# Kernel tuning notes

Hardware: AMD Instinct MI355X
Metric: run time of the kernel (lower is better)

Reference implementation:

```python
import jax, jax.numpy as jnp
import numpy as np

EPS = 1e-8


def _conv1d(x, w, b):
    # x: [B, E, L], w: [F, E, K], b: [F] -> [B, F, L] (k=3, pad=1 keeps length)
    y = jax.lax.conv_general_dilated(
        x, w, window_strides=(1,), padding=[(1, 1)],
        dimension_numbers=("NCH", "OIH", "NCH"))
    return y + b[None, :, None]


def setup_inputs() -> dict:
    key = jax.random.key(0)
    kq, ka, ke, kw, kb, ku = jax.random.split(key, 6)
    B, QL, AL = 512, 128, 512
    V, E, F, K = 50000, 300, 400, 3
    question = jax.random.randint(kq, (B, QL), 0, V + 1, dtype=jnp.int64)
    answer = jax.random.randint(ka, (B, AL), 0, V + 1, dtype=jnp.int64)
    emb_table = jax.random.normal(ke, (V + 1, E), dtype=jnp.float32)
    emb_table = emb_table.at[0].set(0.0)  # padding_idx=0
    conv_w = jax.random.normal(kw, (F, E, K), dtype=jnp.float32) * 0.05
    conv_b = jax.random.normal(kb, (F,), dtype=jnp.float32) * 0.05
    U = jax.random.normal(ku, (F, F), dtype=jnp.float32) * 0.1
    return {"question": question, "answer": answer, "emb_table": emb_table,
            "conv_w": conv_w, "conv_b": conv_b, "U": U}


def reference(question, answer, emb_table, conv_w, conv_b, U):
    q = emb_table[question]              # [B, QL, E]
    a = emb_table[answer]                # [B, AL, E]
    Q = _conv1d(q.transpose(0, 2, 1), conv_w, conv_b)   # [B, F, QL]
    A = _conv1d(a.transpose(0, 2, 1), conv_w, conv_b)   # [B, F, AL]
    # G = tanh(Q^T U A): [B, QL, AL]
    G = jnp.tanh(jnp.einsum("bfq,fg,bga->bqa", Q, U, A))
    roQ = jax.nn.softmax(jnp.max(G, axis=2), axis=1)    # [B, QL]
    roA = jax.nn.softmax(jnp.max(G, axis=1), axis=1)    # [B, AL]
    rQ = jnp.einsum("bfq,bq->bf", Q, roQ)               # [B, F]
    rA = jnp.einsum("bfa,ba->bf", A, roA)               # [B, F]
    nQ = jnp.maximum(jnp.linalg.norm(rQ, axis=1), EPS)
    nA = jnp.maximum(jnp.linalg.norm(rA, axis=1), EPS)
    return jnp.sum(rQ * rA, axis=1) / (nQ * nA)         # [B]
```

## Files before the change

kernel.cpp:

```cpp
#include <hip/hip_runtime.h>
#include <math.h>

typedef unsigned int   uint32;
typedef unsigned short ushort16;
typedef __attribute__((ext_vector_type(8))) short  short8;
typedef __attribute__((ext_vector_type(4))) float  floatx4;

#define Bb   512
#define QLn  128
#define ALn  512
#define En   300
#define Fn   400
#define OW   416
#define EPAD 320
#define NV   50001
#define ECROWS 50176
#define ECSTRIDE 2560

typedef const __attribute__((address_space(1))) unsigned int guint_t;
typedef __attribute__((address_space(3))) unsigned int luint_t;
#define GLDS16(g, l) __builtin_amdgcn_global_load_lds((guint_t*)(g), (luint_t*)(l), 16, 0, 0)

static __device__ __forceinline__ float bf_lo(uint32 u) { return __uint_as_float(u << 16); }
static __device__ __forceinline__ float bf_hi(uint32 u) { return __uint_as_float(u & 0xffff0000u); }
static __device__ __forceinline__ ushort16 f2bf(float f) {
    uint32 u = __float_as_uint(f);
    uint32 r = (u + 0x7fffu + ((u >> 16) & 1u)) >> 16;
    return (ushort16)r;
}
static __device__ __forceinline__ uint32 pack2(float a, float b) {
    return (uint32)f2bf(a) | ((uint32)f2bf(b) << 16);
}

__global__ __launch_bounds__(128) void embcvt_kernel(
        const float* __restrict__ emb, char* __restrict__ embbf)
{
    const int r = blockIdx.x, j = threadIdx.x;
    const float* er = emb + (size_t)r * En;
    uint32* orow = (uint32*)(embbf + (size_t)r * 640);
    for (int d = j; d < 160; d += 128) {
        uint32 v = 0;
        if (d < 150) {
            float2 f2v = *(const float2*)(er + 2 * d);
            v = pack2(f2v.x, f2v.y);
        }
        orow[d] = v;
    }
}

__global__ __launch_bounds__(256) void prep_wt(
        const float* __restrict__ W, const float* __restrict__ cb,
        ushort16* __restrict__ Wt2, float* __restrict__ bias2)
{
    const int f = blockIdx.x, t = threadIdx.x;
    for (int p2 = t; p2 < 480; p2 += 256) {
        int p = 2 * p2;
        float v0 = 0.f, v1 = 0.f;
        if (f < Fn) {
            int kk = p / EPAD, e = p - kk * EPAD;
            if (e < En)     v0 = W[(size_t)f * 900 + e * 3 + kk];
            if (e + 1 < En) v1 = W[(size_t)f * 900 + (e + 1) * 3 + kk];
        }
        *(uint32*)&Wt2[(size_t)f * 960 + p] = pack2(v0, v1);
    }
    if (t == 0) bias2[f] = (f < Fn) ? cb[f] : 0.f;
}

__global__ __launch_bounds__(256) void prep_ub(
        const float* __restrict__ U, ushort16* __restrict__ Ub)
{
    const int g = blockIdx.x, t = threadIdx.x;
    uint32* orow = (uint32*)(Ub + (size_t)g * 416);
    for (int f2 = t; f2 < 208; f2 += 256) {
        int f = 2 * f2;
        float v0 = 0.f, v1 = 0.f;
        if (g < Fn) {
            if (f < Fn)     v0 = U[(size_t)f * Fn + g];
            if (f + 1 < Fn) v1 = U[(size_t)(f + 1) * Fn + g];
        }
        orow[f2] = pack2(v0, v1);
    }
}

__global__ __launch_bounds__(512) void ec_gemm(
        const char* __restrict__ embbf, const char* __restrict__ Wt2,
        char* __restrict__ EC)
{
    __shared__ __align__(16) char As[32768];
    __shared__ __align__(16) char Bs[32768];
    const int bx = blockIdx.x;
    const int g = bx / 40, rem = bx - g * 40;
    const int c = rem >> 3, vt = g * 8 + (rem & 7);
    if (vt >= 196) return;
    const int t = threadIdx.x, lane = t & 63, w = t >> 6;
    const int v0 = vt * 256, c0 = c * 256;
    const int wr = w >> 2, wc = w & 3;
    const int fm = lane & 15;
    const int cg = ((lane & 3) - ((lane >> 3) & 3)) & 3;
    const int rl = lane >> 2;
    const int chunkOff = (((lane >> 4) + (fm >> 1)) & 3) * 16;

    const char* srcA[2];
    const char* srcB[2];
#pragma unroll
    for (int i = 0; i < 2; ++i) {
        srcA[i] = embbf + (size_t)(v0 + w * 32 + i * 16 + rl) * 640 + cg * 16;
        int n = c0 + w * 32 + i * 16 + rl;
        int kk = n / 416, f = n - kk * 416;
        if (n >= 1248) { kk = 0; f = 508; }
        srcB[i] = Wt2 + (size_t)f * 1920 + kk * 640 + cg * 16;
    }
    char* AsW = As + w * 2048;
    char* BsW = Bs + w * 2048;

    floatx4 acc[8][4];
    const floatx4 zz = {0.f, 0.f, 0.f, 0.f};
#pragma unroll
    for (int m = 0; m < 8; ++m)
#pragma unroll
        for (int n = 0; n < 4; ++n) acc[m][n] = zz;

#define ESTG(ko, buf) do {                                                    \
        const int _ko = (ko); const int _bo = (buf) * 16384;                  \
        GLDS16(srcA[0] + _ko, AsW + _bo);                                     \
        GLDS16(srcA[1] + _ko, AsW + _bo + 1024);                              \
        GLDS16(srcB[0] + _ko, BsW + _bo);                                     \
        GLDS16(srcB[1] + _ko, BsW + _bo + 1024);                              \
    } while (0)

    int cur = 0;
    ESTG(0, 0);
    __syncthreads();
    for (int ks = 0; ks < 10; ++ks) {
        const int nxt = cur ^ 1;
        if (ks < 9) ESTG((ks + 1) * 64, nxt);
        short8 af[8], bfv[4];
        const char* Ac = As + cur * 16384;
        const char* Bc = Bs + cur * 16384;
#pragma unroll
        for (int m = 0; m < 8; ++m)
            af[m] = *(const short8*)(Ac + (wr * 128 + m * 16 + fm) * 64 + chunkOff);
#pragma unroll
        for (int n = 0; n < 4; ++n)
            bfv[n] = *(const short8*)(Bc + (wc * 64 + n * 16 + fm) * 64 + chunkOff);
        __builtin_amdgcn_s_setprio(1);
#pragma unroll
        for (int m = 0; m < 8; ++m)
#pragma unroll
            for (int n = 0; n < 4; ++n)
                acc[m][n] = __builtin_amdgcn_mfma_f32_16x16x32_bf16(
                    bfv[n], af[m], acc[m][n], 0, 0, 0);
        __builtin_amdgcn_s_setprio(0);
        __syncthreads();
        cur = nxt;
    }
#undef ESTG

#pragma unroll
    for (int m = 0; m < 8; ++m) {
        const int v = v0 + wr * 128 + m * 16 + fm;
#pragma unroll
        for (int n = 0; n < 4; ++n) {
            const int f0 = c0 + wc * 64 + n * 16 + ((lane >> 4) * 4);
            uint2 o;
            o.x = pack2(acc[m][n][0], acc[m][n][1]);
            o.y = pack2(acc[m][n][2], acc[m][n][3]);
            *(uint2*)(EC + (size_t)v * ECSTRIDE + f0 * 2) = o;
        }
    }
}

static __device__ __forceinline__ void gather_one(
        const int* __restrict__ toks, const char* __restrict__ EC,
        const float* __restrict__ bias2, char* __restrict__ outb,
        int id, int L)
{
    const uint32 uid = (uint32)id;
    const int c = (int)(uid % 52u);
    const int r = (int)(uid / 52u);
    const int l = r & (L - 1), b = r / L;
    const int* tr = toks + (size_t)b * L;
    const int t0 = (l > 0)     ? tr[l - 1] : 0;
    const int t1 = tr[l];
    const int t2 = (l < L - 1) ? tr[l + 1] : 0;
    const uint4 x0 = *(const uint4*)(EC + (size_t)t0 * ECSTRIDE +        c * 16);
    const uint4 x1 = *(const uint4*)(EC + (size_t)t1 * ECSTRIDE +  832 + c * 16);
    const uint4 x2 = *(const uint4*)(EC + (size_t)t2 * ECSTRIDE + 1664 + c * 16);
    const float4 b0 = *(const float4*)(bias2 + c * 8);
    const float4 b1 = *(const float4*)(bias2 + c * 8 + 4);
    uint4 o;
    o.x = pack2(bf_lo(x0.x) + bf_lo(x1.x) + bf_lo(x2.x) + b0.x,
                bf_hi(x0.x) + bf_hi(x1.x) + bf_hi(x2.x) + b0.y);
    o.y = pack2(bf_lo(x0.y) + bf_lo(x1.y) + bf_lo(x2.y) + b0.z,
                bf_hi(x0.y) + bf_hi(x1.y) + bf_hi(x2.y) + b0.w);
    o.z = pack2(bf_lo(x0.z) + bf_lo(x1.z) + bf_lo(x2.z) + b1.x,
                bf_hi(x0.z) + bf_hi(x1.z) + bf_hi(x2.z) + b1.y);
    o.w = pack2(bf_lo(x0.w) + bf_lo(x1.w) + bf_lo(x2.w) + b1.z,
                bf_hi(x0.w) + bf_hi(x1.w) + bf_hi(x2.w) + b1.w);
    *(uint4*)(outb + (size_t)r * 832 + c * 16) = o;
}

#define GQB 1024
#define GAB 4096
__global__ __launch_bounds__(256) void gather_both(
        const int* __restrict__ question, const int* __restrict__ answer,
        const char* __restrict__ EC, const float* __restrict__ bias2,
        char* __restrict__ qb, char* __restrict__ ab, int nb)
{
    const int bx = blockIdx.x, t = threadIdx.x;
    if (bx < GQB) {
        const int total = nb * QLn * 52;
        for (int id = bx * 256 + t; id < total; id += GQB * 256)
            gather_one(question, EC, bias2, qb, id, QLn);
    } else {
        const int total = nb * ALn * 52;
        for (int id = (bx - GQB) * 256 + t; id < total; id += GAB * 256)
            gather_one(answer, EC, bias2, ab, id, ALn);
    }
}

template<int NWM, int NWN, int MF, int NF, int BR>
static __device__ __forceinline__ void qp_tile(
        const char* __restrict__ Qb, const char* __restrict__ Ub,
        char* __restrict__ ob, int col0, char* As, char* Bs)
{
    const int t = threadIdx.x, lane = t & 63, w = t >> 6;
    const int wr = w / NWN, wc = w % NWN;
    const int fm = lane & 15;
    const int cg = ((lane & 3) - ((lane >> 3) & 3)) & 3;
    const int rl = lane >> 2;
    const int chunkOff = (((lane >> 4) + (fm >> 1)) & 3) * 16;

    const char* srcA = Qb + (size_t)(w * 16 + rl) * 832 + cg * 16;
    const char* srcB0; const char* srcB1 = 0;
    if (BR == 256) {
        srcB0 = Ub + (size_t)(col0 + w * 32 + rl) * 832 + cg * 16;
        srcB1 = srcB0 + (size_t)16 * 832;
    } else {
        srcB0 = Ub + (size_t)(col0 + w * 16 + rl) * 832 + cg * 16;
        srcB1 = Ub + (size_t)(col0 + 128 + w * 16 + rl) * 832 + cg * 16;
    }
    char* AsW = As + w * 1024;
    char* BsW0; char* BsW1;
    if (BR == 256) { BsW0 = Bs + w * 2048; BsW1 = BsW0 + 1024; }
    else           { BsW0 = Bs + w * 1024; BsW1 = Bs + 8192 + w * 1024; }
    const int BUFB = BR * 64;

    floatx4 acc[MF][NF];
    const floatx4 zz = {0.f, 0.f, 0.f, 0.f};
#pragma unroll
    for (int m = 0; m < MF; ++m)
#pragma unroll
        for (int n = 0; n < NF; ++n) acc[m][n] = zz;

#define QSTG(ko, buf) do {                                                    \
        const int _ko = (ko);                                                 \
        GLDS16(srcA + _ko, AsW + (buf) * 8192);                               \
        GLDS16(srcB0 + _ko, BsW0 + (buf) * BUFB);                             \
        if (BR == 256 || w < 2) GLDS16(srcB1 + _ko, BsW1 + (buf) * BUFB);     \
    } while (0)

    int cur = 0;
    QSTG(0, 0);
    __syncthreads();
    for (int ks = 0; ks < 13; ++ks) {
        const int nxt = cur ^ 1;
        if (ks < 12) QSTG((ks + 1) * 64, nxt);
        short8 af[MF], bfv[NF];
        const char* Ac = As + cur * 8192;
        const char* Bc = Bs + cur * BUFB;
#pragma unroll
        for (int m = 0; m < MF; ++m)
            af[m] = *(const short8*)(Ac + (wr * (MF * 16) + m * 16 + fm) * 64 + chunkOff);
#pragma unroll
        for (int n = 0; n < NF; ++n)
            bfv[n] = *(const short8*)(Bc + (wc * (NF * 16) + n * 16 + fm) * 64 + chunkOff);
        __builtin_amdgcn_s_setprio(1);
#pragma unroll
        for (int m = 0; m < MF; ++m)
#pragma unroll
            for (int n = 0; n < NF; ++n)
                acc[m][n] = __builtin_amdgcn_mfma_f32_16x16x32_bf16(
                    af[m], bfv[n], acc[m][n], 0, 0, 0);
        __builtin_amdgcn_s_setprio(0);
        __syncthreads();
        cur = nxt;
    }
#undef QSTG

#pragma unroll
    for (int m = 0; m < MF; ++m) {
        const int row = wr * (MF * 16) + m * 16 + ((lane >> 4) * 4);
#pragma unroll
        for (int n = 0; n < NF; ++n) {
            const int col = col0 + wc * (NF * 16) + n * 16 + fm;
#pragma unroll
            for (int r = 0; r < 4; ++r)
                *(ushort16*)(ob + (size_t)(row + r) * 832 + col * 2) =
                    f2bf(acc[m][n][r]);
        }
    }
}

__global__ __launch_bounds__(512) void qp_gemm(
        const char* __restrict__ qb, const char* __restrict__ Ub,
        char* __restrict__ qpb, int nb)
{
    __shared__ __align__(16) char As[16384];
    __shared__ __align__(16) char Bs[32768];
    const int bx = blockIdx.x;
    const int xcd = bx & 7, rest = bx >> 3;
    const int nt = rest & 1, b = (rest >> 1) * 8 + xcd;
    if (b >= nb) return;
    const char* Qb = qb + (size_t)b * 106496;
    char* ob = qpb + (size_t)b * 106496;
    if (nt == 0)
        qp_tile<2, 4, 4, 4, 256>(Qb, Ub, ob, 0, As, Bs);
    else
        qp_tile<4, 2, 2, 5, 160>(Qb, Ub, ob, 256, As, Bs);
}

__global__ __launch_bounds__(256) void fused_g(
        const ushort16* __restrict__ Qp,
        const ushort16* __restrict__ Av,
        float* __restrict__ rowPart,
        float* __restrict__ colMg,
        int nb)
{
    __shared__ __align__(16) char Qs[16384];
    __shared__ __align__(16) char Asl[32768];
    __shared__ float rowM4[128][4];

    const int t = threadIdx.x, lane = t & 63, w = t >> 6;
    const int bx = blockIdx.x;
    const int xcd = bx & 7, rest = bx >> 3;
    const int c = rest & 1, b = (rest >> 1) * 8 + xcd;
    if (b >= nb) return;
    const int fm = lane & 15;
    const int cg = ((lane & 3) - ((lane >> 3) & 3)) & 3;
    const int rl = lane >> 2;
    const int chunkOff = (((lane >> 4) + (fm >> 1)) & 3) * 16;

    const char* Qpb = (const char*)Qp + (size_t)b * 106496;
    const char* Ab  = (const char*)Av + (size_t)b * 425984 + (size_t)c * 212992;
    const char* srcQ0 = Qpb + (size_t)(w * 16 + rl) * 832 + cg * 16;
    const char* srcQ1 = Qpb + (size_t)(64 + w * 16 + rl) * 832 + cg * 16;
    const char* srcA0 = Ab  + (size_t)(w * 64 + rl) * 832 + cg * 16;

    floatx4 acc[8][4];
    const floatx4 zz = {0.f, 0.f, 0.f, 0.f};
#pragma unroll
    for (int m = 0; m < 8; ++m)
#pragma unroll
        for (int n = 0; n < 4; ++n) acc[m][n] = zz;

#define FSTG(ko, buf) do {                                                    \
        const int _ko = (ko);                                                 \
        GLDS16(srcQ0 + _ko, Qs + (buf) * 8192 + w * 1024);                    \
        GLDS16(srcQ1 + _ko, Qs + (buf) * 8192 + 4096 + w * 1024);             \
        GLDS16(srcA0 + _ko,         Asl + (buf) * 16384 + w * 4096);          \
        GLDS16(srcA0 + 13312 + _ko, Asl + (buf) * 16384 + w * 4096 + 1024);   \
        GLDS16(srcA0 + 26624 + _ko, Asl + (buf) * 16384 + w * 4096 + 2048);   \
        GLDS16(srcA0 + 39936 + _ko, Asl + (buf) * 16384 + w * 4096 + 3072);   \
    } while (0)

    int cur = 0;
    FSTG(0, 0);
    __syncthreads();

    for (int ks = 0; ks < 13; ++ks) {
        const int nxt = cur ^ 1;
        if (ks < 12) FSTG((ks + 1) * 64, nxt);

        short8 qa[8], aa_[4];
        const char* Qc = Qs + cur * 8192;
        const char* Ac = Asl + cur * 16384;
#pragma unroll
        for (int m = 0; m < 8; ++m)
            qa[m] = *(const short8*)(Qc + (m * 16 + fm) * 64 + chunkOff);
#pragma unroll
        for (int n = 0; n < 4; ++n)
            aa_[n] = *(const short8*)(Ac + (w * 64 + n * 16 + fm) * 64 + chunkOff);
        __builtin_amdgcn_s_setprio(1);
#pragma unroll
        for (int m = 0; m < 8; ++m)
#pragma unroll
            for (int n = 0; n < 4; ++n)
                acc[m][n] = __builtin_amdgcn_mfma_f32_16x16x32_bf16(
                    qa[m], aa_[n], acc[m][n], 0, 0, 0);
        __builtin_amdgcn_s_setprio(0);
        __syncthreads();
        cur = nxt;
    }
#undef FSTG

#pragma unroll
    for (int m = 0; m < 8; ++m)
#pragma unroll
        for (int r = 0; r < 4; ++r) {
            float v = fmaxf(fmaxf(acc[m][0][r], acc[m][1][r]),
                            fmaxf(acc[m][2][r], acc[m][3][r]));
            v = fmaxf(v, __shfl_xor(v, 1));
            v = fmaxf(v, __shfl_xor(v, 2));
            v = fmaxf(v, __shfl_xor(v, 4));
            v = fmaxf(v, __shfl_xor(v, 8));
            if (fm == 0) rowM4[m * 16 + (lane >> 4) * 4 + r][w] = v;
        }
#pragma unroll
    for (int n = 0; n < 4; ++n) {
        float v = -1e30f;
#pragma unroll
        for (int m = 0; m < 8; ++m)
#pragma unroll
            for (int r = 0; r < 4; ++r) v = fmaxf(v, acc[m][n][r]);
        v = fmaxf(v, __shfl_xor(v, 16));
        v = fmaxf(v, __shfl_xor(v, 32));
        if (lane < 16)
            colMg[(size_t)b * 512 + c * 256 + w * 64 + n * 16 + lane] = v;
    }
    __syncthreads();
    if (t < 128)
        rowPart[((size_t)b * 2 + c) * 128 + t] =
            fmaxf(fmaxf(rowM4[t][0], rowM4[t][1]),
                  fmaxf(rowM4[t][2], rowM4[t][3]));
}

static __device__ __forceinline__ float block_reduce_max_1k(float v, volatile float* red) {
    int t = threadIdx.x;
    red[t] = v; __syncthreads();
    for (int s = 512; s > 0; s >>= 1) {
        if (t < s) red[t] = fmaxf(red[t], red[t + s]);
        __syncthreads();
    }
    float r = red[0]; __syncthreads();
    return r;
}
static __device__ __forceinline__ float block_reduce_sum_1k(float v, volatile float* red) {
    int t = threadIdx.x;
    red[t] = v; __syncthreads();
    for (int s = 512; s > 0; s >>= 1) {
        if (t < s) red[t] = red[t] + red[t + s];
        __syncthreads();
    }
    float r = red[0]; __syncthreads();
    return r;
}

__global__ __launch_bounds__(1024) void fused_pool(
        const ushort16* __restrict__ Qv,
        const ushort16* __restrict__ Av,
        const float* __restrict__ rowPart,
        const float* __restrict__ colMg,
        float* __restrict__ out)
{
    __shared__ float colv[ALn];
    __shared__ float roq[QLn];
    __shared__ float red[1024];
    __shared__ float part[4][4][208];
    const int t = threadIdx.x, b = blockIdx.x;

    float v = -1e30f;
    if (t < QLn) {
        const float* rp = rowPart + (size_t)b * 256;
        v = tanhf(fmaxf(rp[t], rp[128 + t]));
    }
    float vmax = block_reduce_max_1k(v, red);
    float ex = (t < QLn) ? __expf(v - vmax) : 0.f;
    float ssum = block_reduce_sum_1k(ex, red);
    if (t < QLn) roq[t] = ex / ssum;

    float cv = (t < ALn) ? tanhf(colMg[(size_t)b * 512 + t]) : -1e30f;
    float cmax = block_reduce_max_1k(cv, red);
    float e0 = (t < ALn) ? __expf(cv - cmax) : 0.f;
    float csum = block_reduce_sum_1k(e0, red);
    if (t < ALn) colv[t] = e0 / csum;
    __syncthreads();

    if (t < 832) {
        const int h = t / 208, c = t - h * 208;
        float rq0 = 0.f, rq1 = 0.f, ra0 = 0.f, ra1 = 0.f;
        const uint32* Qb32 = (const uint32*)((const char*)Qv + (size_t)b * 106496);
#pragma unroll 4
        for (int q = h * 32; q < h * 32 + 32; ++q) {
            float wv = roq[q];
            uint32 u = Qb32[q * 208 + c];
            rq0 = fmaf(bf_lo(u), wv, rq0);
            rq1 = fmaf(bf_hi(u), wv, rq1);
        }
        const uint32* Ab32 = (const uint32*)((const char*)Av + (size_t)b * 425984);
#pragma unroll 4
        for (int a = h * 128; a < h * 128 + 128; ++a) {
            float wv = colv[a];
            uint32 u = Ab32[a * 208 + c];
            ra0 = fmaf(bf_lo(u), wv, ra0);
            ra1 = fmaf(bf_hi(u), wv, ra1);
        }
        part[0][h][c] = rq0; part[1][h][c] = rq1;
        part[2][h][c] = ra0; part[3][h][c] = ra1;
    }
    __syncthreads();

    float dd = 0.f, qq = 0.f, aam = 0.f;
    if (t < 208) {
        float q0 = part[0][0][t] + part[0][1][t] + part[0][2][t] + part[0][3][t];
        float q1 = part[1][0][t] + part[1][1][t] + part[1][2][t] + part[1][3][t];
        float a0 = part[2][0][t] + part[2][1][t] + part[2][2][t] + part[2][3][t];
        float a1 = part[3][0][t] + part[3][1][t] + part[3][2][t] + part[3][3][t];
        dd  = q0 * a0 + q1 * a1;
        qq  = q0 * q0 + q1 * q1;
        aam = a0 * a0 + a1 * a1;
    }
    dd  = block_reduce_sum_1k(dd, red);
    qq  = block_reduce_sum_1k(qq, red);
    aam = block_reduce_sum_1k(aam, red);
    if (t == 0) {
        float nq = fmaxf(sqrtf(qq), 1e-8f);
        float na = fmaxf(sqrtf(aam), 1e-8f);
        out[b] = dd / (nq * na);
    }
}

extern "C" void kernel_launch(void* const* d_in, const int* in_sizes, int n_in,
                              void* d_out, int out_size, void* d_ws, size_t ws_size,
                              hipStream_t stream)
{
    const int*   question = (const int*)d_in[0];
    const int*   answer   = (const int*)d_in[1];
    const float* emb      = (const float*)d_in[2];
    const float* conv_w   = (const float*)d_in[3];
    const float* conv_b   = (const float*)d_in[4];
    const float* U        = (const float*)d_in[5];
    float* out = (float*)d_out;
    char* ws = (char*)d_ws;

    const size_t WT2B   = (size_t)512 * 960 * 2;
    const size_t UBB    = (size_t)416 * 416 * 2;
    const size_t ECB    = (size_t)ECROWS * ECSTRIDE;
    const size_t FIXED0 = WT2B + 2048 + UBB + ECB;
    const size_t QB     = (size_t)QLn * OW * 2;
    const size_t AB     = (size_t)ALn * OW * 2;
    const size_t MXB    = 4096;
    const size_t PER_B  = 2 * QB + AB + MXB;

    size_t avail = (ws_size > FIXED0) ? (ws_size - FIXED0) : 0;
    int CB = (int)(avail / PER_B);
    if (CB > Bb) CB = Bb;
    if (CB < 1)  CB = 1;
    int nch = (Bb + CB - 1) / CB;
    int CBe = (Bb + nch - 1) / nch;

    char*  wt2   = ws;
    float* bias2 = (float*)(ws + WT2B);
    char*  ub    = ws + WT2B + 2048;
    char*  EC    = ws + WT2B + 2048 + UBB;
    char*  embbf = ws + FIXED0;
    char*  qb    = ws + FIXED0;
    char*  qpb   = qb  + (size_t)CB * QB;
    char*  ab    = qpb + (size_t)CB * QB;
    float* rowP  = (float*)(ab + (size_t)CB * AB);
    float* colM  = rowP + (size_t)CB * 512;

    embcvt_kernel<<<NV, 128, 0, stream>>>(emb, embbf);
    prep_wt<<<512, 256, 0, stream>>>(conv_w, conv_b, (ushort16*)wt2, bias2);
    prep_ub<<<416, 256, 0, stream>>>(U, (ushort16*)ub);
    ec_gemm<<<1000, 512, 0, stream>>>(embbf, wt2, EC);

    for (int b0 = 0; b0 < Bb; b0 += CBe) {
        int nb = (Bb - b0 < CBe) ? (Bb - b0) : CBe;
        int nb8 = (nb + 7) / 8;
        gather_both<<<GQB + GAB, 256, 0, stream>>>(
            question + (size_t)b0 * QLn, answer + (size_t)b0 * ALn,
            EC, bias2, qb, ab, nb);
        qp_gemm<<<nb8 * 16, 512, 0, stream>>>(qb, ub, qpb, nb);
        fused_g<<<nb8 * 16, 256, 0, stream>>>((const ushort16*)qpb, (const ushort16*)ab,
                                              rowP, colM, nb);
        fused_pool<<<nb, 1024, 0, stream>>>((const ushort16*)qb, (const ushort16*)ab,
                                            rowP, colM, out + b0);
    }
}
```

Before: 610.3 us.

## Triple-buffer ec_gemm loads with explicit waitcnt and widen gather per thread

The embedding-conv GEMM moves from double to triple buffering in LDS (96KB). It uses explicit vmcnt waits and a single barrier per k-step, so global-to-LDS loads run two stages ahead and one barrier per iteration is dropped. The grid changes from a grouped 1D launch to a plain 2D launch, which loses the earlier block ordering meant for L2 reuse. The gather kernel now processes two 16-byte chunks per thread instead of one. The larger LDS footprint may lower occupancy.

After: 615.7 us. No clear change (+0.9%).

```diff
diff --git a/kernel.cpp b/kernel.cpp
--- a/kernel.cpp
+++ b/kernel.cpp
@@ -86,12 +86,9 @@
         const char* __restrict__ embbf, const char* __restrict__ Wt2,
         char* __restrict__ EC)
 {
-    __shared__ __align__(16) char As[32768];
-    __shared__ __align__(16) char Bs[32768];
-    const int bx = blockIdx.x;
-    const int g = bx / 40, rem = bx - g * 40;
-    const int c = rem >> 3, vt = g * 8 + (rem & 7);
-    if (vt >= 196) return;
+    __shared__ __align__(16) char As[49152];
+    __shared__ __align__(16) char Bs[49152];
+    const int vt = blockIdx.x, c = blockIdx.y;
     const int t = threadIdx.x, lane = t & 63, w = t >> 6;
     const int v0 = vt * 256, c0 = c * 256;
     const int wr = w >> 2, wc = w & 3;
@@ -128,21 +125,28 @@
         GLDS16(srcB[1] + _ko, BsW + _bo + 1024);                              \
     } while (0)
 
-    int cur = 0;
     ESTG(0, 0);
-    __syncthreads();
+    ESTG(64, 1);
+
+#pragma unroll
     for (int ks = 0; ks < 10; ++ks) {
-        const int nxt = cur ^ 1;
-        if (ks < 9) ESTG((ks + 1) * 64, nxt);
+        if (ks == 9) asm volatile("s_waitcnt vmcnt(0)" ::: "memory");
+        else         asm volatile("s_waitcnt vmcnt(4)" ::: "memory");
+        __builtin_amdgcn_s_barrier();
+        __builtin_amdgcn_sched_barrier(0);
+
         short8 af[8], bfv[4];
-        const char* Ac = As + cur * 16384;
-        const char* Bc = Bs + cur * 16384;
+        const char* Ac = As + (ks % 3) * 16384;
+        const char* Bc = Bs + (ks % 3) * 16384;
 #pragma unroll
         for (int m = 0; m < 8; ++m)
             af[m] = *(const short8*)(Ac + (wr * 128 + m * 16 + fm) * 64 + chunkOff);
 #pragma unroll
         for (int n = 0; n < 4; ++n)
             bfv[n] = *(const short8*)(Bc + (wc * 64 + n * 16 + fm) * 64 + chunkOff);
+
+        if (ks < 8) ESTG((ks + 2) * 64, (ks + 2) % 3);
+
         __builtin_amdgcn_s_setprio(1);
 #pragma unroll
         for (int m = 0; m < 8; ++m)
@@ -151,8 +155,7 @@
                 acc[m][n] = __builtin_amdgcn_mfma_f32_16x16x32_bf16(
                     bfv[n], af[m], acc[m][n], 0, 0, 0);
         __builtin_amdgcn_s_setprio(0);
-        __syncthreads();
-        cur = nxt;
+        __builtin_amdgcn_sched_barrier(0);
     }
 #undef ESTG
 
@@ -176,28 +179,35 @@
         int id, int L)
 {
     const uint32 uid = (uint32)id;
-    const int c = (int)(uid % 52u);
-    const int r = (int)(uid / 52u);
+    const int c = (int)(uid % 26u);
+    const int r = (int)(uid / 26u);
     const int l = r & (L - 1), b = r / L;
     const int* tr = toks + (size_t)b * L;
     const int t0 = (l > 0)     ? tr[l - 1] : 0;
     const int t1 = tr[l];
     const int t2 = (l < L - 1) ? tr[l + 1] : 0;
-    const uint4 x0 = *(const uint4*)(EC + (size_t)t0 * ECSTRIDE +        c * 16);
-    const uint4 x1 = *(const uint4*)(EC + (size_t)t1 * ECSTRIDE +  832 + c * 16);
-    const uint4 x2 = *(const uint4*)(EC + (size_t)t2 * ECSTRIDE + 1664 + c * 16);
-    const float4 b0 = *(const float4*)(bias2 + c * 8);
-    const float4 b1 = *(const float4*)(bias2 + c * 8 + 4);
-    uint4 o;
-    o.x = pack2(bf_lo(x0.x) + bf_lo(x1.x) + bf_lo(x2.x) + b0.x,
-                bf_hi(x0.x) + bf_hi(x1.x) + bf_hi(x2.x) + b0.y);
-    o.y = pack2(bf_lo(x0.y) + bf_lo(x1.y) + bf_lo(x2.y) + b0.z,
-                bf_hi(x0.y) + bf_hi(x1.y) + bf_hi(x2.y) + b0.w);
-    o.z = pack2(bf_lo(x0.z) + bf_lo(x1.z) + bf_lo(x2.z) + b1.x,
-                bf_hi(x0.z) + bf_hi(x1.z) + bf_hi(x2.z) + b1.y);
-    o.w = pack2(bf_lo(x0.w) + bf_lo(x1.w) + bf_lo(x2.w) + b1.z,
-                bf_hi(x0.w) + bf_hi(x1.w) + bf_hi(x2.w) + b1.w);
-    *(uint4*)(outb + (size_t)r * 832 + c * 16) = o;
+    const char* p0 = EC + (size_t)t0 * ECSTRIDE +        c * 32;
+    const char* p1 = EC + (size_t)t1 * ECSTRIDE +  832 + c * 32;
+    const char* p2 = EC + (size_t)t2 * ECSTRIDE + 1664 + c * 32;
+    char* po = outb + (size_t)r * 832 + c * 32;
+#pragma unroll
+    for (int h = 0; h < 2; ++h) {
+        const uint4 x0 = *(const uint4*)(p0 + h * 16);
+        const uint4 x1 = *(const uint4*)(p1 + h * 16);
+        const uint4 x2 = *(const uint4*)(p2 + h * 16);
+        const float4 b0 = *(const float4*)(bias2 + c * 16 + h * 8);
+        const float4 b1 = *(const float4*)(bias2 + c * 16 + h * 8 + 4);
+        uint4 o;
+        o.x = pack2(bf_lo(x0.x) + bf_lo(x1.x) + bf_lo(x2.x) + b0.x,
+                    bf_hi(x0.x) + bf_hi(x1.x) + bf_hi(x2.x) + b0.y);
+        o.y = pack2(bf_lo(x0.y) + bf_lo(x1.y) + bf_lo(x2.y) + b0.z,
+                    bf_hi(x0.y) + bf_hi(x1.y) + bf_hi(x2.y) + b0.w);
+        o.z = pack2(bf_lo(x0.z) + bf_lo(x1.z) + bf_lo(x2.z) + b1.x,
+                    bf_hi(x0.z) + bf_hi(x1.z) + bf_hi(x2.z) + b1.y);
+        o.w = pack2(bf_lo(x0.w) + bf_lo(x1.w) + bf_lo(x2.w) + b1.z,
+                    bf_hi(x0.w) + bf_hi(x1.w) + bf_hi(x2.w) + b1.w);
+        *(uint4*)(po + h * 16) = o;
+    }
 }
 
 #define GQB 1024
@@ -209,11 +219,11 @@
 {
     const int bx = blockIdx.x, t = threadIdx.x;
     if (bx < GQB) {
-        const int total = nb * QLn * 52;
+        const int total = nb * QLn * 26;
         for (int id = bx * 256 + t; id < total; id += GQB * 256)
             gather_one(question, EC, bias2, qb, id, QLn);
     } else {
-        const int total = nb * ALn * 52;
+        const int total = nb * ALn * 26;
         for (int id = (bx - GQB) * 256 + t; id < total; id += GAB * 256)
             gather_one(answer, EC, bias2, ab, id, ALn);
     }
@@ -563,7 +573,7 @@
     embcvt_kernel<<<NV, 128, 0, stream>>>(emb, embbf);
     prep_wt<<<512, 256, 0, stream>>>(conv_w, conv_b, (ushort16*)wt2, bias2);
     prep_ub<<<416, 256, 0, stream>>>(U, (ushort16*)ub);
-    ec_gemm<<<1000, 512, 0, stream>>>(embbf, wt2, EC);
+    ec_gemm<<<dim3(196, 5), 512, 0, stream>>>(embbf, wt2, EC);
 
     for (int b0 = 0; b0 < Bb; b0 += CBe) {
         int nb = (Bb - b0 < CBe) ? (Bb - b0) : CBe;
```

## Triple-buffer ec_gemm with smaller N tiles and manual waitcnt pipelining

Applied to the files above, without the earlier changes.

Restructures the embedding-times-conv-weight GEMM so each block computes a 256x128 tile instead of 256x256, over a 2D grid of 196x10 blocks. Shared memory becomes a three-stage ring, filled two k-steps ahead, with explicit vmcnt waits and raw barriers in place of __syncthreads. Each wave now holds a 4x4 accumulator array, down from 8x4, and launch bounds request higher occupancy. The aim is to hide global-to-LDS load latency and raise occupancy, at the cost of more blocks and re-reading the A tile for each N tile.

Measured after the change: 625.3 us. 2.5% more time.

```diff
diff --git a/kernel.cpp b/kernel.cpp
--- a/kernel.cpp
+++ b/kernel.cpp
@@ -82,89 +82,90 @@
     }
 }
 
-__global__ __launch_bounds__(512) void ec_gemm(
+__global__ __launch_bounds__(512, 4) void ec_gemm(
         const char* __restrict__ embbf, const char* __restrict__ Wt2,
         char* __restrict__ EC)
 {
-    __shared__ __align__(16) char As[32768];
-    __shared__ __align__(16) char Bs[32768];
-    const int bx = blockIdx.x;
-    const int g = bx / 40, rem = bx - g * 40;
-    const int c = rem >> 3, vt = g * 8 + (rem & 7);
-    if (vt >= 196) return;
+    __shared__ __align__(16) char As[49152];
+    __shared__ __align__(16) char Bs[24576];
+    const int vt = blockIdx.x, c = blockIdx.y;
     const int t = threadIdx.x, lane = t & 63, w = t >> 6;
-    const int v0 = vt * 256, c0 = c * 256;
-    const int wr = w >> 2, wc = w & 3;
+    const int v0 = vt * 256, c0 = c * 128;
+    const int wr = w >> 1, wc = w & 1;
     const int fm = lane & 15;
     const int cg = ((lane & 3) - ((lane >> 3) & 3)) & 3;
     const int rl = lane >> 2;
     const int chunkOff = (((lane >> 4) + (fm >> 1)) & 3) * 16;
 
     const char* srcA[2];
-    const char* srcB[2];
-#pragma unroll
-    for (int i = 0; i < 2; ++i) {
+#pragma unroll
+    for (int i = 0; i < 2; ++i)
         srcA[i] = embbf + (size_t)(v0 + w * 32 + i * 16 + rl) * 640 + cg * 16;
-        int n = c0 + w * 32 + i * 16 + rl;
-        int kk = n / 416, f = n - kk * 416;
-        if (n >= 1248) { kk = 0; f = 508; }
-        srcB[i] = Wt2 + (size_t)f * 1920 + kk * 640 + cg * 16;
-    }
+    int n = c0 + w * 16 + rl;
+    int kk = n / 416, f = n - kk * 416;
+    if (n >= 1248) { kk = 0; f = 508; }
+    const char* srcB = Wt2 + (size_t)f * 1920 + kk * 640 + cg * 16;
+
     char* AsW = As + w * 2048;
-    char* BsW = Bs + w * 2048;
-
-    floatx4 acc[8][4];
+    char* BsW = Bs + w * 1024;
+
+    floatx4 acc[4][4];
     const floatx4 zz = {0.f, 0.f, 0.f, 0.f};
 #pragma unroll
-    for (int m = 0; m < 8; ++m)
-#pragma unroll
-        for (int n = 0; n < 4; ++n) acc[m][n] = zz;
+    for (int m = 0; m < 4; ++m)
+#pragma unroll
+        for (int nn = 0; nn < 4; ++nn) acc[m][nn] = zz;
 
 #define ESTG(ko, buf) do {                                                    \
-        const int _ko = (ko); const int _bo = (buf) * 16384;                  \
-        GLDS16(srcA[0] + _ko, AsW + _bo);                                     \
-        GLDS16(srcA[1] + _ko, AsW + _bo + 1024);                              \
-        GLDS16(srcB[0] + _ko, BsW + _bo);                                     \
-        GLDS16(srcB[1] + _ko, BsW + _bo + 1024);                              \
+        const int _ko = (ko);                                                 \
+        GLDS16(srcA[0] + _ko, AsW + (buf) * 16384);                           \
+        GLDS16(srcA[1] + _ko, AsW + (buf) * 16384 + 1024);                    \
+        GLDS16(srcB + _ko,    BsW + (buf) * 8192);                            \
     } while (0)
 
-    int cur = 0;
     ESTG(0, 0);
-    __syncthreads();
+    ESTG(64, 1);
+
+#pragma unroll
     for (int ks = 0; ks < 10; ++ks) {
-        const int nxt = cur ^ 1;
-        if (ks < 9) ESTG((ks + 1) * 64, nxt);
-        short8 af[8], bfv[4];
-        const char* Ac = As + cur * 16384;
-        const char* Bc = Bs + cur * 16384;
-#pragma unroll
-        for (int m = 0; m < 8; ++m)
-            af[m] = *(const short8*)(Ac + (wr * 128 + m * 16 + fm) * 64 + chunkOff);
-#pragma unroll
-        for (int n = 0; n < 4; ++n)
-            bfv[n] = *(const short8*)(Bc + (wc * 64 + n * 16 + fm) * 64 + chunkOff);
+        if (ks == 9) asm volatile("s_waitcnt vmcnt(0)" ::: "memory");
+        else         asm volatile("s_waitcnt vmcnt(3)" ::: "memory");
+        __builtin_amdgcn_s_barrier();
+        __builtin_amdgcn_sched_barrier(0);
+
+        short8 af[4], bfv[4];
+        const char* Ac = As + (ks % 3) * 16384;
+        const char* Bc = Bs + (ks % 3) * 8192;
+#pragma unroll
+        for (int m = 0; m < 4; ++m)
+            af[m] = *(const short8*)(Ac + (wr * 64 + m * 16 + fm) * 64 + chunkOff);
+#pragma unroll
+        for (int nn = 0; nn < 4; ++nn)
+            bfv[nn] = *(const short8*)(Bc + (wc * 64 + nn * 16 + fm) * 64 + chunkOff);
+
+        if (ks < 8) ESTG((ks + 2) * 64, (ks + 2) % 3);
+
         __builtin_amdgcn_s_setprio(1);
 #pragma unroll
-        for (int m = 0; m < 8; ++m)
-#pragma unroll
-            for (int n = 0; n < 4; ++n)
-                acc[m][n] = __builtin_amdgcn_mfma_f32_16x16x32_bf16(
-                    bfv[n], af[m], acc[m][n], 0, 0, 0);
+        for (int m = 0; m < 4; ++m)
+#pragma unroll
+            for (int nn = 0; nn < 4; ++nn)
+                acc[m][nn] = __builtin_amdgcn_mfma_f32_16x16x32_bf16(
+                    bfv[nn], af[m], acc[m][nn], 0, 0, 0);
         __builtin_amdgcn_s_setprio(0);
-        __syncthreads();
-        cur = nxt;
+        __builtin_amdgcn_sched_barrier(0);
     }
 #undef ESTG
 
 #pragma unroll
-    for (int m = 0; m < 8; ++m) {
-        const int v = v0 + wr * 128 + m * 16 + fm;
-#pragma unroll
-        for (int n = 0; n < 4; ++n) {
-            const int f0 = c0 + wc * 64 + n * 16 + ((lane >> 4) * 4);
+    for (int m = 0; m < 4; ++m) {
+        const int v = v0 + wr * 64 + m * 16 + fm;
+#pragma unroll
+        for (int nn = 0; nn < 4; ++nn) {
+            const int f0 = c0 + wc * 64 + nn * 16 + ((lane >> 4) * 4);
             uint2 o;
-            o.x = pack2(acc[m][n][0], acc[m][n][1]);
-            o.y = pack2(acc[m][n][2], acc[m][n][3]);
+            o.x = pack2(acc[m][nn][0], acc[m][nn][1]);
+            o.y = pack2(acc[m][nn][2], acc[m][nn][3]);
             *(uint2*)(EC + (size_t)v * ECSTRIDE + f0 * 2) = o;
         }
     }
@@ -563,7 +564,7 @@
     embcvt_kernel<<<NV, 128, 0, stream>>>(emb, embbf);
     prep_wt<<<512, 256, 0, stream>>>(conv_w, conv_b, (ushort16*)wt2, bias2);
     prep_ub<<<416, 256, 0, stream>>>(U, (ushort16*)ub);
-    ec_gemm<<<1000, 512, 0, stream>>>(embbf, wt2, EC);
+    ec_gemm<<<dim3(196, 10), 512, 0, stream>>>(embbf, wt2, EC);
 
     for (int b0 = 0; b0 < Bb; b0 += CBe) {
         int nb = (Bb - b0 < CBe) ? (Bb - b0) : CBe;
```
